# Performance work log

Measured on AMD Instinct MI355X. Metric: run time of the kernel, lower is better.

Reference implementation:

```python
import jax, jax.numpy as jnp
import numpy as np

B, S, H = 2, 2048, 2048
NH, NKV, HD = 16, 4, 128
ROPE_BASE = 10000.0


def rotate_half(x):
    x1, x2 = jnp.split(x, 2, axis=-1)
    return jnp.concatenate((-x2, x1), axis=-1)


def setup_inputs() -> dict:
    key = jax.random.key(0)
    ks = jax.random.split(key, 6)
    hidden_states = jax.random.normal(ks[0], (B, S, H), dtype=jnp.float32)
    # additive causal mask, as used by HF: 0 on allowed, large negative on masked
    causal = jnp.triu(jnp.full((S, S), -1e9, dtype=jnp.float32), k=1)
    attention_mask = jnp.broadcast_to(causal[None, None], (B, 1, S, S))
    position_ids = jnp.broadcast_to(jnp.arange(S, dtype=jnp.int64)[None], (B, S))
    scale = 1.0 / np.sqrt(H)
    Wq = jax.random.normal(ks[1], (NH * HD, H), dtype=jnp.float32) * scale
    Wk = jax.random.normal(ks[2], (NKV * HD, H), dtype=jnp.float32) * scale
    Wv = jax.random.normal(ks[3], (NKV * HD, H), dtype=jnp.float32) * scale
    Wo = jax.random.normal(ks[4], (H, NH * HD), dtype=jnp.float32) * scale
    return {"hidden_states": hidden_states, "attention_mask": attention_mask,
            "position_ids": position_ids, "Wq": Wq, "Wk": Wk, "Wv": Wv, "Wo": Wo}


def reference(hidden_states, attention_mask, position_ids, Wq, Wk, Wv, Wo):
    b, s, _ = hidden_states.shape
    # projections (torch Linear: y = x W^T)
    q = jnp.einsum('bsh,oh->bso', hidden_states, Wq).reshape(b, s, NH, HD).transpose(0, 2, 1, 3)
    k = jnp.einsum('bsh,oh->bso', hidden_states, Wk).reshape(b, s, NKV, HD).transpose(0, 2, 1, 3)
    v = jnp.einsum('bsh,oh->bso', hidden_states, Wv).reshape(b, s, NKV, HD).transpose(0, 2, 1, 3)
    # RoPE
    inv_freq = 1.0 / (ROPE_BASE ** (jnp.arange(0, HD, 2, dtype=jnp.float32) / HD))  # [HD/2]
    freqs = position_ids.astype(jnp.float32)[:, :, None] * inv_freq[None, None, :]  # [B,S,HD/2]
    emb = jnp.concatenate((freqs, freqs), axis=-1)                                  # [B,S,HD]
    cos = jnp.cos(emb)[:, None]  # [B,1,S,HD]
    sin = jnp.sin(emb)[:, None]
    q = q * cos + rotate_half(q) * sin
    k = k * cos + rotate_half(k) * sin
    # GQA repeat (repeat_interleave along head axis)
    n_rep = NH // NKV
    k = jnp.repeat(k, n_rep, axis=1)
    v = jnp.repeat(v, n_rep, axis=1)
    scale = HD ** -0.5
    attn = jnp.einsum('bhqd,bhkd->bhqk', q, k) * scale
    attn = attn + attention_mask
    attn = jax.nn.softmax(attn.astype(jnp.float32), axis=-1).astype(q.dtype)
    out = jnp.einsum('bhqk,bhkd->bhqd', attn, v)            # [B,NH,S,HD]
    out = out.transpose(0, 2, 1, 3).reshape(b, s, NH * HD)  # [B,S,H]
    return jnp.einsum('bso,ho->bsh', out, Wo)
```

## Files before the change

kernel.cpp:

```cpp
#include <hip/hip_runtime.h>


#define B_ 2
#define S_ 2048
#define H_ 2048
#define NH_ 16
#define NKV_ 4
#define HD_ 128
#define QKV_N 3072

typedef unsigned short u16;
typedef unsigned int u32;
typedef unsigned long long u64;
typedef __attribute__((ext_vector_type(8))) short short8;
typedef __attribute__((ext_vector_type(4))) float floatx4;
typedef __attribute__((ext_vector_type(16))) float floatx16;

__device__ __forceinline__ u16 f2bf(float f) {
    union { float f; u32 u; } v; v.f = f;
    u32 u = v.u;
    return (u16)((u + 0x7fffu + ((u >> 16) & 1u)) >> 16);
}
__device__ __forceinline__ float bf2f(u16 h) {
    union { u32 u; float f; } v; v.u = ((u32)h) << 16;
    return v.f;
}
__device__ __forceinline__ void store_out(u16* p, float v)  { *p = f2bf(v); }
__device__ __forceinline__ void store_out(float* p, float v) { *p = v; }

__device__ __forceinline__ void gload_lds16(const void* g, void* l) {
    __builtin_amdgcn_global_load_lds(
        (const __attribute__((address_space(1))) void*)g,
        (__attribute__((address_space(3))) void*)l, 16, 0, 0);
}

__device__ __forceinline__ u32 cvtpk(float lo, float hi) {
    u32 r;
    asm("v_cvt_pk_bf16_f32 %0, %1, %2" : "=v"(r) : "v"(lo), "v"(hi));
    return r;
}

__device__ __forceinline__ void pl32swap(u32& a, u32& b) {
#if __has_builtin(__builtin_amdgcn_permlane32_swap)
    typedef __attribute__((ext_vector_type(2))) int iv2;
    iv2 r = __builtin_amdgcn_permlane32_swap((int)a, (int)b, false, false);
    a = (u32)r[0];
    b = (u32)r[1];
#else
    asm volatile("v_permlane32_swap_b32 %0, %1" : "+v"(a), "+v"(b));
#endif
}

__global__ __launch_bounds__(256) void cast_f32_bf16(const float* __restrict__ in,
                                                     u16* __restrict__ out, int n) {
    int i = (blockIdx.x * 256 + threadIdx.x) * 4;
    if (i + 3 < n) {
        float4 f = *(const float4*)(in + i);
        out[i + 0] = f2bf(f.x);
        out[i + 1] = f2bf(f.y);
        out[i + 2] = f2bf(f.z);
        out[i + 3] = f2bf(f.w);
    }
}

template <typename OutT>
__global__ __launch_bounds__(256) void gemm128(const u16* __restrict__ A,
                                               const u16* __restrict__ Bm,
                                               OutT* __restrict__ C,
                                               int M, int N, int K) {
    __shared__ __align__(16) u16 As[128][32];
    __shared__ __align__(16) u16 Bs[128][32];
    const int tid  = threadIdx.x;
    const int wave = tid >> 6;
    const int lane = tid & 63;
    const int quad = lane >> 4;
    const int l16  = lane & 15;
    const int m0 = blockIdx.y * 128;
    const int n0 = blockIdx.x * 128;
    const int wm = (wave >> 1) * 64;
    const int wn = (wave & 1) * 64;
    const int srow = tid >> 2;
    const int scol = (tid & 3) * 8;

    floatx4 acc[4][4] = {};

    for (int k0 = 0; k0 < K; k0 += 32) {
        __syncthreads();
        gload_lds16(A  + (size_t)(m0 + srow) * K + k0 + scol,      &As[srow][scol]);
        gload_lds16(A  + (size_t)(m0 + 64 + srow) * K + k0 + scol, &As[64 + srow][scol]);
        gload_lds16(Bm + (size_t)(n0 + srow) * K + k0 + scol,      &Bs[srow][scol]);
        gload_lds16(Bm + (size_t)(n0 + 64 + srow) * K + k0 + scol, &Bs[64 + srow][scol]);
        __syncthreads();
        short8 af[4], bfv[4];
        for (int i = 0; i < 4; ++i) {
            af[i]  = *(const short8*)&As[wm + i * 16 + l16][quad * 8];
            bfv[i] = *(const short8*)&Bs[wn + i * 16 + l16][quad * 8];
        }
        for (int mi = 0; mi < 4; ++mi)
            for (int ni = 0; ni < 4; ++ni)
                acc[mi][ni] = __builtin_amdgcn_mfma_f32_16x16x32_bf16(
                    af[mi], bfv[ni], acc[mi][ni], 0, 0, 0);
    }
    for (int mi = 0; mi < 4; ++mi)
        for (int ni = 0; ni < 4; ++ni)
            for (int r = 0; r < 4; ++r) {
                int row = m0 + wm + mi * 16 + quad * 4 + r;
                int col = n0 + wn + ni * 16 + l16;
                store_out(C + (size_t)row * N + col, acc[mi][ni][r]);
            }
}

__global__ __launch_bounds__(256) void rope_kernel(u16* buf, int hofs, int nheads,
                                                   int total, float oscale) {
    int i = blockIdx.x * 256 + threadIdx.x;
    if (i >= total) return;
    int d = i & 63;
    int t = i >> 6;
    int head = t % nheads;
    int row  = t / nheads;
    int s    = row & (S_ - 1);
    size_t base = (size_t)row * QKV_N + hofs + head * HD_;
    float invf = exp2f(-(float)d * (13.28771237954945f / 64.0f));
    float fr = (float)s * invf;
    float sn, cs;
    sincosf(fr, &sn, &cs);
    float x1 = bf2f(buf[base + d]);
    float x2 = bf2f(buf[base + d + 64]);
    buf[base + d]      = f2bf((x1 * cs - x2 * sn) * oscale);
    buf[base + d + 64] = f2bf((x2 * cs + x1 * sn) * oscale);
}

__global__ __launch_bounds__(256) void transpose_v(const u16* __restrict__ qkv,
                                                   u16* __restrict__ vt) {
    __shared__ u16 t[32][33];
    const int tx = threadIdx.x, ty = threadIdx.y;
    const int c0 = blockIdx.x * 32, s0 = blockIdx.y * 32, b = blockIdx.z;
    for (int i = 0; i < 4; ++i)
        t[ty + i * 8][tx] =
            qkv[((size_t)(b * S_ + s0 + ty + i * 8)) * QKV_N + 2560 + c0 + tx];
    __syncthreads();
    for (int i = 0; i < 4; ++i)
        vt[((size_t)(b * 512 + c0 + ty + i * 8)) * S_ + s0 + tx] = t[tx][ty + i * 8];
}

__global__ __launch_bounds__(256) void flash_attn(const u16* __restrict__ qkv,
                                                  const u16* __restrict__ vtg,
                                                  u16* __restrict__ o) {
    __shared__ __align__(16) u16 KsL[64 * 128];
    __shared__ __align__(16) u16 VtL[128 * 64];

    const int tid  = threadIdx.x;
    const int wave = tid >> 6;
    const int lane = tid & 63;
    const int l31  = lane & 31;
    const int hi   = lane >> 5;
    const int wq   = wave >> 1;
    const int kb   = wave & 1;

    const int bx = (int)blockIdx.x;
    const int by = (int)blockIdx.y;
    const int flip = (by >> 3) & 1;
    const int a4 = bx & 15;
    const int jq = flip ? a4 : (31 - a4);
    const int bh = (by & 7) | (((by >> 4) & 1) << 3) | ((bx >> 4) << 4);
    const int b   = bh >> 4;
    const int h   = bh & 15;
    const int kvh = h >> 2;
    const int q0  = jq * 64;

    const size_t qb = ((size_t)(b * S_ + q0 + wq * 32 + l31)) * QKV_N + h * HD_;
    short8 qf[8];
#pragma unroll
    for (int mf = 0; mf < 8; ++mf)
        qf[mf] = *(const short8*)(qkv + qb + mf * 16 + hi * 8);

    floatx16 o_acc[4] = {};
    float l_loc = 0.f;

    const size_t kbase = (size_t)(b * S_) * QKV_N + 2048 + kvh * HD_;
    const size_t vbase = (size_t)((b * NKV_ + kvh) * HD_) * S_;
    const int krow_l = (lane >> 4);
    const int kslot  = lane & 15;
    const int vrow_l = (lane >> 3);
    const int vslot  = lane & 7;

    const int rk = kb * 32 + l31;
    const int kswz = rk & 7;

    for (int kt = 0; kt <= jq; ++kt) {
        __syncthreads();
#pragma unroll
        for (int p = 0; p < 4; ++p) {
            int r = 16 * wave + 4 * p + krow_l;
            gload_lds16(qkv + kbase + (size_t)(kt * 64 + r) * QKV_N
                            + ((kslot ^ (r & 7)) * 8),
                        &KsL[(16 * wave + 4 * p) * 128 + lane * 8]);
            int rv = 32 * wave + 8 * p + vrow_l;
            gload_lds16(vtg + vbase + (size_t)rv * S_ + kt * 64
                            + ((vslot ^ (rv & 7)) * 8),
                        &VtL[(32 * wave + 8 * p) * 64 + lane * 8]);
        }
        __syncthreads();

        floatx16 st = {};
#pragma unroll
        for (int mf = 0; mf < 8; ++mf) {
            short8 kf = *(const short8*)&KsL[rk * 128 + (((mf * 2 + hi) ^ kswz) * 8)];
            st = __builtin_amdgcn_mfma_f32_32x32x16_bf16(kf, qf[mf], st, 0, 0, 0);
        }
        if (kt == jq) {
            int qloc = wq * 32 + l31;
#pragma unroll
            for (int r = 0; r < 16; ++r) {
                int krow = kb * 32 + (r & 3) + 8 * (r >> 2) + 4 * hi;
                if (krow > qloc) st[r] = -INFINITY;
            }
        }
        u32 pk[8];
        float ll = 0.f;
#pragma unroll
        for (int i = 0; i < 8; ++i) {
            float e0 = __expf(st[2 * i]);
            float e1 = __expf(st[2 * i + 1]);
            ll += e0 + e1;
            pk[i] = cvtpk(e0, e1);
        }
        l_loc += ll;
        pl32swap(pk[0], pk[2]);
        pl32swap(pk[1], pk[3]);
        pl32swap(pk[4], pk[6]);
        pl32swap(pk[5], pk[7]);
        union { u32 u[4]; short8 s; } c0, c1;
        c0.u[0] = pk[0]; c0.u[1] = pk[1]; c0.u[2] = pk[2]; c0.u[3] = pk[3];
        c1.u[0] = pk[4]; c1.u[1] = pk[5]; c1.u[2] = pk[6]; c1.u[3] = pk[7];
#pragma unroll
        for (int dblk = 0; dblk < 4; ++dblk) {
            int rv = dblk * 32 + l31;
            int sw = rv & 7;
            short8 va = *(const short8*)&VtL[rv * 64 + (((kb * 4 + hi) ^ sw) * 8)];
            o_acc[dblk] = __builtin_amdgcn_mfma_f32_32x32x16_bf16(va, c0.s, o_acc[dblk], 0, 0, 0);
            short8 vb = *(const short8*)&VtL[rv * 64 + (((kb * 4 + 2 + hi) ^ sw) * 8)];
            o_acc[dblk] = __builtin_amdgcn_mfma_f32_32x32x16_bf16(vb, c1.s, o_acc[dblk], 0, 0, 0);
        }
    }

    float lt = l_loc + __shfl_xor(l_loc, 32, 64);
    __syncthreads();
    float* scr = (float*)KsL;
    if (kb == 1) scr[wq * 64 + lane] = lt;
    __syncthreads();
    float linv = 0.f;
    if (kb == 0) linv = 1.0f / (lt + scr[wq * 64 + lane]);

#pragma unroll
    for (int dblk = 0; dblk < 4; ++dblk) {
        __syncthreads();
        if (kb == 1) {
#pragma unroll
            for (int r = 0; r < 16; ++r)
                scr[wq * 1088 + lane * 17 + r] = o_acc[dblk][r];
        }
        __syncthreads();
        if (kb == 0) {
            const int row = q0 + wq * 32 + l31;
#pragma unroll
            for (int rg = 0; rg < 4; ++rg) {
                float v0 = (o_acc[dblk][rg * 4 + 0] + scr[wq * 1088 + lane * 17 + rg * 4 + 0]) * linv;
                float v1 = (o_acc[dblk][rg * 4 + 1] + scr[wq * 1088 + lane * 17 + rg * 4 + 1]) * linv;
                float v2 = (o_acc[dblk][rg * 4 + 2] + scr[wq * 1088 + lane * 17 + rg * 4 + 2]) * linv;
                float v3 = (o_acc[dblk][rg * 4 + 3] + scr[wq * 1088 + lane * 17 + rg * 4 + 3]) * linv;
                u32 wlo = cvtpk(v0, v1);
                u32 whi = cvtpk(v2, v3);
                int col = h * HD_ + dblk * 32 + rg * 8 + 4 * hi;
                u64 pack = (u64)wlo | ((u64)whi << 32);
                *(u64*)(o + ((size_t)(b * S_ + row)) * H_ + col) = pack;
            }
        }
    }
}

extern "C" void kernel_launch(void* const* d_in, const int* in_sizes, int n_in,
                              void* d_out, int out_size, void* d_ws, size_t ws_size,
                              hipStream_t stream) {
    const float* hs = (const float*)d_in[0];
    const float* Wq = (const float*)d_in[3];
    const float* Wk = (const float*)d_in[4];
    const float* Wv = (const float*)d_in[5];
    const float* Wo = (const float*)d_in[6];

    char* ws = (char*)d_ws;
    const size_t MB = 1024 * 1024;
    u16* hs_b   = (u16*)(ws + 0);
    u16* wqkv_b = (u16*)(ws + 16 * MB);
    u16* vt_b   = (u16*)(ws + 16 * MB);
    u16* wo_b   = (u16*)(ws + 28 * MB);
    u16* qkv    = (u16*)(ws + 36 * MB);

    const int M = B_ * S_;

    cast_f32_bf16<<<8192, 256, 0, stream>>>(hs, hs_b, M * H_);
    cast_f32_bf16<<<4096, 256, 0, stream>>>(Wq, wqkv_b, H_ * H_);
    cast_f32_bf16<<<1024, 256, 0, stream>>>(Wk, wqkv_b + 2048 * 2048, 512 * H_);
    cast_f32_bf16<<<1024, 256, 0, stream>>>(Wv, wqkv_b + 2560 * 2048, 512 * H_);
    cast_f32_bf16<<<4096, 256, 0, stream>>>(Wo, wo_b, H_ * H_);

    gemm128<u16><<<dim3(QKV_N / 128, M / 128), 256, 0, stream>>>(
        hs_b, wqkv_b, qkv, M, QKV_N, H_);

    rope_kernel<<<(M * NH_ * 64) / 256, 256, 0, stream>>>(
        qkv, 0, NH_, M * NH_ * 64, 0.08838834764831845f);
    rope_kernel<<<(M * NKV_ * 64) / 256, 256, 0, stream>>>(
        qkv, 2048, NKV_, M * NKV_ * 64, 1.0f);

    transpose_v<<<dim3(16, 64, 2), dim3(32, 8), 0, stream>>>(qkv, vt_b);

    flash_attn<<<dim3(32, 32), 256, 0, stream>>>(qkv, vt_b, hs_b);

    gemm128<float><<<dim3(H_ / 128, M / 128), 256, 0, stream>>>(
        hs_b, wo_b, (float*)d_out, M, H_, H_);
}
```

Baseline: 345.3 us.

## Merge cast and RoPE launches, vectorize bf16 stores, and swizzle GEMM blocks across XCDs

The five f32→bf16 cast launches become one kernel that picks its source tensor by index range, and it packs four bf16 values into a single 64-bit store. The two RoPE launches are merged into one kernel the same way. The GEMM remaps block ids so that consecutive tiles land on the same XCD (8-way chiplet swizzle), which is meant to improve L2 reuse. The changes cut launch overhead and store instruction count, at the cost of a little branch logic per thread.

```diff
diff --git a/kernel.cpp b/kernel.cpp
--- a/kernel.cpp
+++ b/kernel.cpp
@@ -51,16 +51,26 @@
 #endif
 }
 
-__global__ __launch_bounds__(256) void cast_f32_bf16(const float* __restrict__ in,
-                                                     u16* __restrict__ out, int n) {
-    int i = (blockIdx.x * 256 + threadIdx.x) * 4;
-    if (i + 3 < n) {
-        float4 f = *(const float4*)(in + i);
-        out[i + 0] = f2bf(f.x);
-        out[i + 1] = f2bf(f.y);
-        out[i + 2] = f2bf(f.z);
-        out[i + 3] = f2bf(f.w);
-    }
+__global__ __launch_bounds__(256) void cast_all(const float* __restrict__ hs,
+                                                const float* __restrict__ Wq,
+                                                const float* __restrict__ Wk,
+                                                const float* __restrict__ Wv,
+                                                const float* __restrict__ Wo,
+                                                u16* __restrict__ hs_b,
+                                                u16* __restrict__ wqkv_b,
+                                                u16* __restrict__ wo_b) {
+    int q = blockIdx.x * 256 + threadIdx.x;
+    const float* src;
+    u16* dst;
+    if (q < 2097152)      { src = hs; dst = hs_b; }
+    else if (q < 3145728) { q -= 2097152; src = Wq; dst = wqkv_b; }
+    else if (q < 3407872) { q -= 3145728; src = Wk; dst = wqkv_b + 2048 * 2048; }
+    else if (q < 3670016) { q -= 3407872; src = Wv; dst = wqkv_b + 2560 * 2048; }
+    else                  { q -= 3670016; src = Wo; dst = wo_b; }
+    float4 f = ((const float4*)src)[q];
+    u32 lo = ((u32)f2bf(f.y) << 16) | f2bf(f.x);
+    u32 hi2 = ((u32)f2bf(f.w) << 16) | f2bf(f.z);
+    *(u64*)(dst + (size_t)q * 4) = (u64)lo | ((u64)hi2 << 32);
 }
 
 template <typename OutT>
@@ -75,8 +85,17 @@
     const int lane = tid & 63;
     const int quad = lane >> 4;
     const int l16  = lane & 15;
-    const int m0 = blockIdx.y * 128;
-    const int n0 = blockIdx.x * 128;
+
+    const int nbx = gridDim.x, nby = gridDim.y;
+    const int total = nbx * nby;
+    int n = (int)blockIdx.y * nbx + (int)blockIdx.x;
+    if ((total & 7) == 0) {
+        int cpx = total >> 3;
+        n = (n & 7) * cpx + (n >> 3);
+    }
+    const int m0 = (n / nbx) * 128;
+    const int n0 = (n % nbx) * 128;
+
     const int wm = (wave >> 1) * 64;
     const int wn = (wave & 1) * 64;
     const int srow = tid >> 2;
@@ -110,10 +129,12 @@
             }
 }
 
-__global__ __launch_bounds__(256) void rope_kernel(u16* buf, int hofs, int nheads,
-                                                   int total, float oscale) {
+__global__ __launch_bounds__(256) void rope2(u16* buf) {
     int i = blockIdx.x * 256 + threadIdx.x;
-    if (i >= total) return;
+    int hofs, nheads;
+    float oscale;
+    if (i < 4194304) { hofs = 0;    nheads = 16; oscale = 0.08838834764831845f; }
+    else             { i -= 4194304; hofs = 2048; nheads = 4;  oscale = 1.0f; }
     int d = i & 63;
     int t = i >> 6;
     int head = t % nheads;
@@ -298,19 +319,12 @@
 
     const int M = B_ * S_;
 
-    cast_f32_bf16<<<8192, 256, 0, stream>>>(hs, hs_b, M * H_);
-    cast_f32_bf16<<<4096, 256, 0, stream>>>(Wq, wqkv_b, H_ * H_);
-    cast_f32_bf16<<<1024, 256, 0, stream>>>(Wk, wqkv_b + 2048 * 2048, 512 * H_);
-    cast_f32_bf16<<<1024, 256, 0, stream>>>(Wv, wqkv_b + 2560 * 2048, 512 * H_);
-    cast_f32_bf16<<<4096, 256, 0, stream>>>(Wo, wo_b, H_ * H_);
+    cast_all<<<18432, 256, 0, stream>>>(hs, Wq, Wk, Wv, Wo, hs_b, wqkv_b, wo_b);
 
     gemm128<u16><<<dim3(QKV_N / 128, M / 128), 256, 0, stream>>>(
         hs_b, wqkv_b, qkv, M, QKV_N, H_);
 
-    rope_kernel<<<(M * NH_ * 64) / 256, 256, 0, stream>>>(
-        qkv, 0, NH_, M * NH_ * 64, 0.08838834764831845f);
-    rope_kernel<<<(M * NKV_ * 64) / 256, 256, 0, stream>>>(
-        qkv, 2048, NKV_, M * NKV_ * 64, 1.0f);
+    rope2<<<20480, 256, 0, stream>>>(qkv);
 
     transpose_v<<<dim3(16, 64, 2), dim3(32, 8), 0, stream>>>(qkv, vt_b);
 
```

Measured after the change: 332.6 us. 3.7% less time.
